# Optimization experiments

Hardware: AMD Instinct MI355X
Metric: run time of the kernel (lower is better)

Reference implementation:

```python
import jax, jax.numpy as jnp
import numpy as np

V = 32000   # vocab
D = 1024    # dim
H = 16      # query heads
HKV = 8     # kv heads (GQA)
DH = D // H # head dim = 64
L = 2       # layers
FF = 3584   # expert hidden dim
E = 8       # experts
K = 2       # top-k
EPS = 1e-5
BASE = 1000000.0
B, S = 1, 2048


def setup_inputs() -> dict:
    key = jax.random.key(0)
    ks = jax.random.split(key, 10)
    s = 0.02
    return {
        "x": jax.random.randint(ks[0], (B, S), 0, V, dtype=jnp.int64) if jax.config.jax_enable_x64 else jax.random.randint(ks[0], (B, S), 0, V),
        "emb": jax.random.normal(ks[1], (V, D), jnp.float32) * s,
        "ln_w": jnp.ones((L, D), jnp.float32),
        "ffln_w": jnp.ones((L, D), jnp.float32),
        "wq": jax.random.normal(ks[2], (L, D, H * DH), jnp.float32) * s,
        "wk": jax.random.normal(ks[3], (L, D, HKV * DH), jnp.float32) * s,
        "wv": jax.random.normal(ks[4], (L, D, HKV * DH), jnp.float32) * s,
        "wo": jax.random.normal(ks[5], (L, H * DH, D), jnp.float32) * s,
        "gate_w": jax.random.normal(ks[6], (L, E, D), jnp.float32) * s,
        "w1": jax.random.normal(ks[7], (L, E, FF, D), jnp.float32) * s,
        "w2": jax.random.normal(ks[8], (L, E, D, FF), jnp.float32) * s,
        "w3": jax.random.normal(ks[9], (L, E, FF, D), jnp.float32) * s,
        "dec_norm_w": jnp.ones((D,), jnp.float32),
    }


def rmsnorm(x, w):
    # LayerNormParameterized(use_mean=False, shift=False) == RMSNorm, pow in fp32
    xf = x.astype(jnp.float32)
    var = jnp.mean(xf * xf, axis=-1, keepdims=True)
    return ((xf * jax.lax.rsqrt(var + EPS)).astype(x.dtype)) * w


def rope(xh, pos):
    # interleaved (complex-pair) rotary embedding, xh: [B, S, h, DH]
    half = DH // 2
    freqs = 1.0 / (BASE ** (jnp.arange(0, half, dtype=jnp.float32) * 2.0 / DH))
    ang = pos[:, None] * freqs[None, :]                       # [S, half]
    cos = jnp.cos(ang)[None, :, None, :]
    sin = jnp.sin(ang)[None, :, None, :]
    x1 = xh[..., 0::2]
    x2 = xh[..., 1::2]
    out = jnp.stack([x1 * cos - x2 * sin, x1 * sin + x2 * cos], axis=-1)
    return out.reshape(xh.shape)


def reference(x, emb, ln_w, ffln_w, wq, wk, wv, wo, gate_w, w1, w2, w3, dec_norm_w):
    h = emb[x]                                                # [B, S, D]
    pos = jnp.arange(S, dtype=jnp.float32)
    causal = jnp.tril(jnp.ones((S, S), bool))[None, None]     # [1,1,S,S]
    scale = 1.0 / np.sqrt(DH).astype(np.float32)
    for i in range(L):
        # --- attention sub-layer ---
        res = h
        xn = rmsnorm(h, ln_w[i])
        q = rope((xn @ wq[i]).reshape(B, S, H, DH), pos)
        k = rope((xn @ wk[i]).reshape(B, S, HKV, DH), pos)
        v = (xn @ wv[i]).reshape(B, S, HKV, DH)
        rep = H // HKV
        k = jnp.repeat(k, rep, axis=2)                        # [B,S,H,DH]
        v = jnp.repeat(v, rep, axis=2)
        scores = jnp.einsum('bqhd,bkhd->bhqk', q, k) * scale
        scores = jnp.where(causal, scores, jnp.float32(-1e9))
        att = jax.nn.softmax(scores, axis=-1)
        o = jnp.einsum('bhqk,bkhd->bqhd', att, v).reshape(B, S, H * DH) @ wo[i]
        h = res + o
        # --- MoE FFN sub-layer ---
        res = h
        xn = rmsnorm(h, ffln_w[i]).reshape(B * S, D)          # [T, D]
        logits = xn @ gate_w[i].T                             # [T, E]
        gates = jax.nn.softmax(logits, axis=-1)
        topw, topi = jax.lax.top_k(gates, K)                  # [T, K]
        topw = topw / jnp.sum(topw, axis=-1, keepdims=True)
        # dense combine weights [T, E] (zero for unselected experts)
        cw = jnp.einsum('tk,tke->te', topw, jax.nn.one_hot(topi, E, dtype=topw.dtype))
        y = jnp.zeros_like(xn)
        for e in range(E):                                    # fixed small expert loop
            ye = (jax.nn.silu(xn @ w1[i, e].T) * (xn @ w3[i, e].T)) @ w2[i, e].T
            y = y + cw[:, e:e + 1] * ye
        h = res + y.reshape(B, S, D)
    return rmsnorm(h, dec_norm_w)
```

## Files before the change

### kernel.cpp

```cpp
#include <hip/hip_runtime.h>

using u16 = unsigned short;
using u32 = unsigned int;

#define TT 2048
#define DM 1024
#define NH 16
#define NKV 8
#define DHD 64
#define FFD 3584
#define NE 8

typedef __bf16 bf16x8 __attribute__((ext_vector_type(8)));
typedef float f32x4 __attribute__((ext_vector_type(4)));

__device__ __forceinline__ u16 f2bf(float x){
  return __builtin_bit_cast(u16, (__bf16)x);
}
__device__ __forceinline__ float bf2f(u16 h){
  return (float)__builtin_bit_cast(__bf16, h);
}
__device__ __forceinline__ f32x4 mfma16(bf16x8 a, bf16x8 b, f32x4 c){
  return __builtin_amdgcn_mfma_f32_16x16x32_bf16(a, b, c, 0, 0, 0);
}
__device__ __forceinline__ uint4 packhi8v(float4 a, float4 b){
  u16 h0=f2bf(a.x),h1=f2bf(a.y),h2=f2bf(a.z),h3=f2bf(a.w);
  u16 h4=f2bf(b.x),h5=f2bf(b.y),h6=f2bf(b.z),h7=f2bf(b.w);
  return make_uint4((u32)h0|((u32)h1<<16),(u32)h2|((u32)h3<<16),
                    (u32)h4|((u32)h5<<16),(u32)h6|((u32)h7<<16));
}
__device__ __forceinline__ uint4 packlo8v(float4 a, float4 b){
  u16 l0=f2bf(a.x-bf2f(f2bf(a.x))),l1=f2bf(a.y-bf2f(f2bf(a.y)));
  u16 l2=f2bf(a.z-bf2f(f2bf(a.z))),l3=f2bf(a.w-bf2f(f2bf(a.w)));
  u16 l4=f2bf(b.x-bf2f(f2bf(b.x))),l5=f2bf(b.y-bf2f(f2bf(b.y)));
  u16 l6=f2bf(b.z-bf2f(f2bf(b.z))),l7=f2bf(b.w-bf2f(f2bf(b.w)));
  return make_uint4((u32)l0|((u32)l1<<16),(u32)l2|((u32)l3<<16),
                    (u32)l4|((u32)l5<<16),(u32)l6|((u32)l7<<16));
}

#define SWZR(r) ((((r)>>1) ^ ((r)>>3)) & 3)
#define SWC(r,c) ((((c) ^ SWZR(r))) * 8)

__device__ __forceinline__ void glds16(const u16* g, u16* l){
  __builtin_amdgcn_global_load_lds(
      (const __attribute__((address_space(1))) void*)g,
      (__attribute__((address_space(3))) void*)l,
      16, 0, 0);
}

__global__ __launch_bounds__(256) void k_embed(const int* __restrict__ x,
    const float* __restrict__ emb, float* __restrict__ h){
  int t = blockIdx.x;
  int d = threadIdx.x * 4;
  float4 v = *reinterpret_cast<const float4*>(emb + (size_t)x[t] * DM + d);
  *reinterpret_cast<float4*>(h + (size_t)t * DM + d) = v;
}

template<int OUTF32>
__global__ __launch_bounds__(256) void k_rmsnorm(const float* __restrict__ in,
    const float* __restrict__ w, u16* __restrict__ oh, u16* __restrict__ ol,
    float* __restrict__ of){
  int t = blockIdx.x;
  int d4 = threadIdx.x * 4;
  float4 xv = *reinterpret_cast<const float4*>(in + (size_t)t * DM + d4);
  float ss = xv.x*xv.x + xv.y*xv.y + xv.z*xv.z + xv.w*xv.w;
#pragma unroll
  for (int m = 1; m < 64; m <<= 1) ss += __shfl_xor(ss, m);
  __shared__ float sred[4];
  if ((threadIdx.x & 63) == 0) sred[threadIdx.x >> 6] = ss;
  __syncthreads();
  float tot = sred[0] + sred[1] + sred[2] + sred[3];
  float r = 1.0f / sqrtf(tot * (1.0f / DM) + 1e-5f);
  float vv[4] = {xv.x, xv.y, xv.z, xv.w};
#pragma unroll
  for (int jj = 0; jj < 4; jj++){
    float xn = (vv[jj] * r) * w[d4 + jj];
    size_t a = (size_t)t * DM + d4 + jj;
    if constexpr (OUTF32){
      of[a] = xn;
    } else {
      u16 hi = f2bf(xn);
      oh[a] = hi;
      ol[a] = f2bf(xn - bf2f(hi));
    }
  }
}

__global__ __launch_bounds__(256) void k_trig(float* __restrict__ ct, float* __restrict__ st){
  int idx = blockIdx.x * 256 + threadIdx.x;
  int j = idx & 31;
  int s = idx >> 5;
  float xe = (float)j * 0.03125f;
  float yf = (float)pow(1.0e6, (double)xe);
  float fr = 1.0f / yf;
  float ang = (float)s * fr;
  double ad = (double)ang;
  ct[idx] = (float)cos(ad);
  st[idx] = (float)sin(ad);
}

template<int NHD>
__global__ __launch_bounds__(256) void k_rope(const float* __restrict__ in,
    const float* __restrict__ ct, const float* __restrict__ st,
    u16* __restrict__ oh, u16* __restrict__ ol){
  int idx = blockIdx.x * 256 + threadIdx.x;
  int j = idx & 31;
  int hd = (idx >> 5) % NHD;
  int s = idx / (32 * NHD);
  size_t base = ((size_t)s * NHD + hd) * 64 + 2 * j;
  float x1 = in[base], x2 = in[base + 1];
  int ti = (s << 5) | j;
  float c  = ct[ti];
  float sn = st[ti];
  float o1 = x1 * c - x2 * sn;
  float o2 = x1 * sn + x2 * c;
  u16 h1 = f2bf(o1), h2 = f2bf(o2);
  oh[base]     = h1; ol[base]     = f2bf(o1 - bf2f(h1));
  oh[base + 1] = h2; ol[base + 1] = f2bf(o2 - bf2f(h2));
}

__global__ __launch_bounds__(256) void k_splitbuf(const float* __restrict__ in,
    u16* __restrict__ oh, u16* __restrict__ ol, int n){
  int i = blockIdx.x * 256 + threadIdx.x;
  if (i < n){
    float x = in[i];
    u16 hi = f2bf(x);
    oh[i] = hi;
    ol[i] = f2bf(x - bf2f(hi));
  }
}

__global__ __launch_bounds__(256) void k_gate(const u16* __restrict__ xh,
    const u16* __restrict__ xl, const float* __restrict__ gw,
    int* __restrict__ topi, float* __restrict__ topw, int* __restrict__ cnt){
  int wv = threadIdx.x >> 6, lane = threadIdx.x & 63;
  int t = blockIdx.x * 4 + wv;
  float x[16];
#pragma unroll
  for (int i = 0; i < 16; i++){
    size_t a = (size_t)t * DM + lane + 64 * i;
    x[i] = bf2f(xh[a]) + bf2f(xl[a]);
  }
  float lgt[8];
#pragma unroll
  for (int e = 0; e < 8; e++){
    float s = 0.f;
#pragma unroll
    for (int i = 0; i < 16; i++) s += x[i] * gw[(size_t)e * DM + lane + 64 * i];
#pragma unroll
    for (int m = 1; m < 64; m <<= 1) s += __shfl_xor(s, m);
    lgt[e] = s;
  }
  float mx = lgt[0];
#pragma unroll
  for (int e = 1; e < 8; e++) mx = fmaxf(mx, lgt[e]);
  float p[8]; float sum = 0.f;
#pragma unroll
  for (int e = 0; e < 8; e++){ p[e] = expf(lgt[e] - mx); sum += p[e]; }
  float g[8];
#pragma unroll
  for (int e = 0; e < 8; e++) g[e] = p[e] / sum;
  int t0 = 0; float b0 = g[0];
#pragma unroll
  for (int e = 1; e < 8; e++) if (g[e] > b0){ b0 = g[e]; t0 = e; }
  int t1 = -1; float b1 = -1.f;
#pragma unroll
  for (int e = 0; e < 8; e++) if (e != t0 && g[e] > b1){ b1 = g[e]; t1 = e; }
  float ssum = b0 + b1;
  float w0 = b0 / ssum, w1 = b1 / ssum;
  if (lane == 0 && t < TT){
    topi[2*t] = t0; topi[2*t+1] = t1;
    topw[2*t] = w0; topw[2*t+1] = w1;
    atomicAdd(&cnt[t0], 1);
    atomicAdd(&cnt[t1], 1);
  }
}

__global__ void k_zero8(int* cnt){ if (threadIdx.x < 8) cnt[threadIdx.x] = 0; }

__global__ void k_scan(const int* __restrict__ cnt, int* __restrict__ offp, int* __restrict__ cur){
  if (threadIdx.x == 0){
    int r = 0;
    for (int e = 0; e < 8; e++){ offp[e] = r; r += cnt[e]; }
  }
  if (threadIdx.x < 8) cur[threadIdx.x] = 0;
}

__global__ __launch_bounds__(256) void k_scatter(const int* __restrict__ topi,
    const float* __restrict__ topw, const int* __restrict__ offp, int* __restrict__ cur,
    int* __restrict__ ftok, float* __restrict__ fwt){
  int t = blockIdx.x * 256 + threadIdx.x;
  if (t < TT){
#pragma unroll
    for (int j = 0; j < 2; j++){
      int e = topi[2*t + j];
      int p = atomicAdd(&cur[e], 1);
      ftok[offp[e] + p] = t;
      fwt[offp[e] + p] = topw[2*t + j];
    }
  }
}

#define GLDSA(BUF, KK) do { \
    glds16(Ah + gaA0 + (KK), (u16*)&Ash[BUF][awr0][0]); \
    glds16(Ah + gaA1 + (KK), (u16*)&Ash[BUF][awr1][0]); \
    if constexpr (SPLIT){ \
      glds16(Al + gaA0 + (KK), (u16*)&Asl[BUF][awr0][0]); \
      glds16(Al + gaA1 + (KK), (u16*)&Asl[BUF][awr1][0]); \
    } \
  } while(0)

#define GPRELOADB(S, KK) do { \
    if constexpr (BLAYOUT == 0){ \
      const float* bp_ = Bw + (size_t)(n0 + br0) * K + (KK) + cb8; \
      S##B0 = *reinterpret_cast<const float4*>(bp_); \
      S##B1 = *reinterpret_cast<const float4*>(bp_ + 4); \
      if constexpr (TN == 128){ \
        const float* bp2_ = Bw + (size_t)(n0 + br1) * K + (KK) + cb8; \
        S##B2 = *reinterpret_cast<const float4*>(bp2_); \
        S##B3 = *reinterpret_cast<const float4*>(bp2_ + 4); \
      } \
      if constexpr (DUAL){ \
        const float* bq_ = B3w + (size_t)(n0 + br0) * K + (KK) + cb8; \
        S##B2 = *reinterpret_cast<const float4*>(bq_); \
        S##B3 = *reinterpret_cast<const float4*>(bq_ + 4); \
      } \
    } else { \
      S##B0 = *reinterpret_cast<const float4*>(Bw + (size_t)((KK) + kk1) * Nq + n0 + nn1); \
      S##B1 = *reinterpret_cast<const float4*>(Bw + (size_t)((KK) + 16 + kk1) * Nq + n0 + nn1); \
    } \
  } while(0)

#define GSTOREB(S) do { \
    if constexpr (BLAYOUT == 0){ \
      *reinterpret_cast<uint4*>(&Bh1[br0][swB0]) = packhi8v(S##B0, S##B1); \
      if constexpr (SPLIT) *reinterpret_cast<uint4*>(&Bl1[br0][swB0]) = packlo8v(S##B0, S##B1); \
      if constexpr (TN == 128){ \
        *reinterpret_cast<uint4*>(&Bh1[br1][swB1]) = packhi8v(S##B2, S##B3); \
        if constexpr (SPLIT) *reinterpret_cast<uint4*>(&Bl1[br1][swB1]) = packlo8v(S##B2, S##B3); \
      } \
      if constexpr (DUAL){ \
        *reinterpret_cast<uint4*>(&Bh3[br0][swB0]) = packhi8v(S##B2, S##B3); \
        if constexpr (SPLIT) *reinterpret_cast<uint4*>(&Bl3[br0][swB0]) = packlo8v(S##B2, S##B3); \
      } \
    } else { \
      const float* q0 = reinterpret_cast<const float*>(&S##B0); \
      const float* q1 = reinterpret_cast<const float*>(&S##B1); \
      const int ch0 = kk1 >> 3, off0 = kk1 & 7; \
      _Pragma("unroll") \
      for (int j = 0; j < 4; j++){ \
        int row = nn1 + j; \
        int c0 = SWC(row, ch0) + off0; \
        int c1 = SWC(row, ch0 + 2) + off0; \
        u16 h0 = f2bf(q0[j]); \
        Bh1[row][c0] = h0; \
        if constexpr (SPLIT) Bl1[row][c0] = f2bf(q0[j] - bf2f(h0)); \
        u16 h1 = f2bf(q1[j]); \
        Bh1[row][c1] = h1; \
        if constexpr (SPLIT) Bl1[row][c1] = f2bf(q1[j] - bf2f(h1)); \
      } \
    } \
  } while(0)

#define WAITN() do { \
    if constexpr (NBLD == 4) asm volatile("s_waitcnt vmcnt(4) lgkmcnt(0)" ::: "memory"); \
    else                     asm volatile("s_waitcnt vmcnt(2) lgkmcnt(0)" ::: "memory"); \
  } while(0)
#define WAIT0() asm volatile("s_waitcnt vmcnt(0) lgkmcnt(0)" ::: "memory")

#define MFMA_PHASE(CURB) do { \
    bf16x8 af[4], afl[4]; \
    _Pragma("unroll") \
    for (int m = 0; m < 4; m++){ \
      int Ra = wr*64 + m*16 + lr; \
      int sa = SWC(Ra, lg); \
      af[m] = *reinterpret_cast<const bf16x8*>(&Ash[CURB][Ra][sa]); \
      if constexpr (SPLIT) \
        afl[m] = *reinterpret_cast<const bf16x8*>(&Asl[CURB][Ra][sa]); \
    } \
    _Pragma("unroll") \
    for (int n = 0; n < NF; n++){ \
      int Rb = wc*(TN/2) + n*16 + lr; \
      int sb = SWC(Rb, lg); \
      bf16x8 b1 = *reinterpret_cast<const bf16x8*>(&Bh1[Rb][sb]); \
      _Pragma("unroll") \
      for (int m = 0; m < 4; m++) acc[m][n] = mfma16(af[m], b1, acc[m][n]); \
      if constexpr (SPLIT){ \
        bf16x8 bl = *reinterpret_cast<const bf16x8*>(&Bl1[Rb][sb]); \
        _Pragma("unroll") \
        for (int m = 0; m < 4; m++){ \
          acc[m][n] = mfma16(af[m], bl, acc[m][n]); \
          acc[m][n] = mfma16(afl[m], b1, acc[m][n]); \
        } \
      } \
      if constexpr (DUAL){ \
        bf16x8 b3 = *reinterpret_cast<const bf16x8*>(&Bh3[Rb][sb]); \
        _Pragma("unroll") \
        for (int m = 0; m < 4; m++) acc3[m][n] = mfma16(af[m], b3, acc3[m][n]); \
        if constexpr (SPLIT){ \
          bf16x8 b3l = *reinterpret_cast<const bf16x8*>(&Bl3[Rb][sb]); \
          _Pragma("unroll") \
          for (int m = 0; m < 4; m++){ \
            acc3[m][n] = mfma16(af[m], b3l, acc3[m][n]); \
            acc3[m][n] = mfma16(afl[m], b3, acc3[m][n]); \
          } \
        } \
      } \
    } \
  } while(0)

template<int BLAYOUT, int EPI, int SPLIT, int DUAL, int TN, int KS>
__global__ __launch_bounds__(256) void k_gemm(
    const u16* __restrict__ Ah, const u16* __restrict__ Al,
    const float* __restrict__ Bw, const float* __restrict__ B3w,
    const float* __restrict__ Bw2, const float* __restrict__ Bw3,
    size_t strideB, int N, int K,
    float* __restrict__ Cf, int ldc,
    float* __restrict__ Cf2, float* __restrict__ Cf3,
    u16* __restrict__ Ch, u16* __restrict__ Cl,
    const int* __restrict__ cntp, const int* __restrict__ offp,
    const int* __restrict__ ftok, const float* __restrict__ fwt)
{
  static_assert(!(DUAL && TN != 64), "DUAL uses TN=64");
  static_assert(!(BLAYOUT == 1 && TN != 64), "BLAYOUT=1 uses TN=64");
  constexpr int NBLD = (BLAYOUT == 0 && (DUAL || TN == 128)) ? 4 : 2;
  int cnt = TT, off = 0, ks = 0;
  if constexpr (EPI == 2 || EPI == 3){
    int e = blockIdx.z / KS;
    ks = blockIdx.z % KS;
    cnt = cntp[e]; off = offp[e];
    if ((int)blockIdx.y * 128 >= cnt) return;
    Bw += (size_t)e * strideB;
    if constexpr (DUAL) B3w += (size_t)e * strideB;
  } else if constexpr (KS > 1){
    ks = blockIdx.z;
  }
  __shared__ u16 Ash[2][128][32];
  __shared__ u16 Asl[SPLIT ? 2 : 1][SPLIT ? 128 : 1][32];
  __shared__ u16 Bh1[TN][32];
  __shared__ u16 Bl1[SPLIT ? TN : 1][32];
  __shared__ u16 Bh3[DUAL ? TN : 1][32];
  __shared__ u16 Bl3[(DUAL && SPLIT) ? TN : 1][32];

  const int tid = threadIdx.x;
  const int m0 = blockIdx.y * 128;

  int n0, Nq = N, ldq = ldc;
  float* Cq = Cf;
  if constexpr (EPI == 4){
    int bx = blockIdx.x;
    if (bx < 16){       n0 = bx * 64;        Nq = 1024; ldq = 1024; Cq = Cf;  }
    else if (bx < 24){  n0 = (bx - 16) * 64; Nq = 512;  ldq = 512;  Cq = Cf2; Bw = Bw2; }
    else {              n0 = (bx - 24) * 64; Nq = 512;  ldq = 512;  Cq = Cf3; Bw = Bw3; }
  } else {
    n0 = blockIdx.x * TN;
  }

  const int wid = tid >> 6, lane = tid & 63;
  const int wr = wid >> 1, wc = wid & 1;
  const int lr = lane & 15, lg = lane >> 4;
  constexpr int NF = TN / 32;

  const int awr0 = wid * 32;
  const int awr1 = wid * 32 + 16;
  const int rA0 = awr0 + (lane >> 2);
  const int rA1 = awr1 + (lane >> 2);
  const int cA0 = (lane & 3) ^ SWZR(rA0);
  const int cA1 = (lane & 3) ^ SWZR(rA1);
  int grA0, grA1;
  {
    int g0 = m0 + rA0, g1 = m0 + rA1;
    if constexpr (EPI == 2){
      grA0 = ftok[off + (g0 < cnt ? g0 : cnt - 1)];
      grA1 = ftok[off + (g1 < cnt ? g1 : cnt - 1)];
    } else if constexpr (EPI == 3){
      grA0 = off + (g0 < cnt ? g0 : cnt - 1);
      grA1 = off + (g1 < cnt ? g1 : cnt - 1);
    } else {
      grA0 = g0; grA1 = g1;
    }
  }
  const size_t gaA0 = (size_t)grA0 * K + cA0 * 8;
  const size_t gaA1 = (size_t)grA1 * K + cA1 * 8;

  const int br0 = tid >> 2;
  const int br1 = br0 + 64;
  const int cb8 = (tid & 3) * 8;
  const int swB0 = SWC(br0, tid & 3), swB1 = SWC(br1, tid & 3);
  const int kk1 = tid >> 4;
  const int nn1 = (tid & 15) * 4;

  f32x4 acc[4][NF];
  f32x4 acc3[DUAL ? 4 : 1][NF];
#pragma unroll
  for (int m = 0; m < 4; m++)
#pragma unroll
    for (int n = 0; n < NF; n++){
      acc[m][n] = f32x4{0.f,0.f,0.f,0.f};
      if constexpr (DUAL) acc3[m][n] = f32x4{0.f,0.f,0.f,0.f};
    }

  float4 aB0{}, aB1{}, aB2{}, aB3{};
  float4 bB0{}, bB1{}, bB2{}, bB3{};

  const int kbeg = ks * (K / KS);
  const int kend = kbeg + (K / KS);

  GLDSA(0, kbeg);
  GPRELOADB(a, kbeg);
  if (kbeg + 32 < kend) GPRELOADB(b, kbeg + 32);
  int cur = 0;
  for (int k0 = kbeg; k0 < kend; k0 += 64){
    {
      const bool pre = (k0 + 64 < kend);
      GSTOREB(a);
      if (pre) WAITN(); else WAIT0();
      __builtin_amdgcn_s_barrier();
      if (k0 + 32 < kend) GLDSA(cur ^ 1, k0 + 32);
      if (pre) GPRELOADB(a, k0 + 64);
      MFMA_PHASE(cur);
      __builtin_amdgcn_s_barrier();
      cur ^= 1;
    }
    if (k0 + 32 < kend){
      const bool pre = (k0 + 96 < kend);
      GSTOREB(b);
      if (pre) WAITN(); else WAIT0();
      __builtin_amdgcn_s_barrier();
      if (k0 + 64 < kend) GLDSA(cur ^ 1, k0 + 64);
      if (pre) GPRELOADB(b, k0 + 96);
      MFMA_PHASE(cur);
      __builtin_amdgcn_s_barrier();
      cur ^= 1;
    }
  }

#pragma unroll
  for (int m = 0; m < 4; m++)
#pragma unroll
    for (int n = 0; n < NF; n++)
#pragma unroll
      for (int r = 0; r < 4; r++){
        int row = m0 + wr*64 + m*16 + lg*4 + r;
        int col = n0 + wc*(TN/2) + n*16 + lr;
        float v = acc[m][n][r];
        if constexpr (EPI == 0){
          Cf[(size_t)row * ldc + col] = v;
        } else if constexpr (EPI == 1){
          if constexpr (KS > 1) atomicAdd(&Cf[(size_t)row * ldc + col], v);
          else                  Cf[(size_t)row * ldc + col] += v;
        } else if constexpr (EPI == 2){
          if (row < cnt){
            float a3 = acc3[m][n][r];
            float s = v / (1.0f + expf(-v));
            float y = s * a3;
            u16 hi = f2bf(y);
            size_t oa = (size_t)(off + row) * ldc + col;
            Ch[oa] = hi;
            Cl[oa] = f2bf(y - bf2f(hi));
          }
        } else if constexpr (EPI == 3){
          if (row < cnt){
            int tok = ftok[off + row];
            float wgt = fwt[off + row];
            atomicAdd(&Cf[(size_t)tok * ldc + col], wgt * v);
          }
        } else {
          if constexpr (KS > 1) atomicAdd(&Cq[(size_t)row * ldq + col], v);
          else                  Cq[(size_t)row * ldq + col] = v;
        }
      }
}

__global__ __launch_bounds__(256) void k_attn(
    const u16* __restrict__ qh, const u16* __restrict__ ql,
    const u16* __restrict__ kh, const u16* __restrict__ kl,
    const u16* __restrict__ vh, const u16* __restrict__ vl,
    u16* __restrict__ aoh, u16* __restrict__ aol)
{
  const int h  = blockIdx.y;
  const int q0 = blockIdx.x * 64;
  const int hk = h >> 1;
  const int tid = threadIdx.x;
  const int wv = tid >> 6, lane = tid & 63;
  const int lr = lane & 15, lg = lane >> 4;
  const int qw0 = q0 + wv * 16;

  __shared__ u16 Khs[32][72], Kls[32][72];
  __shared__ u16 Vhs[64][40], Vls[64][40];
  __shared__ u16 Phs[4][16][40], Pls[4][16][40];

  bf16x8 qfh[2], qfl[2];
#pragma unroll
  for (int dc = 0; dc < 2; dc++){
    size_t qa = ((size_t)(qw0 + lr) * NH + h) * 64 + dc*32 + lg*8;
    qfh[dc] = *reinterpret_cast<const bf16x8*>(qh + qa);
    qfl[dc] = *reinterpret_cast<const bf16x8*>(ql + qa);
  }
  f32x4 oacc[4];
  float mrun[4], lrun[4];
#pragma unroll
  for (int r = 0; r < 4; r++){ mrun[r] = -1e30f; lrun[r] = 0.f; }
#pragma unroll
  for (int g = 0; g < 4; g++) oacc[g] = f32x4{0.f,0.f,0.f,0.f};

  const int nt = q0 / 32 + 2;
  for (int kt = 0; kt < nt; kt++){
    int kg = kt * 32;
    {
      int kk = tid >> 3, c8 = (tid & 7) * 8;
      size_t ka = ((size_t)(kg + kk) * NKV + hk) * 64 + c8;
      *reinterpret_cast<uint4*>(&Khs[kk][c8]) = *reinterpret_cast<const uint4*>(kh + ka);
      *reinterpret_cast<uint4*>(&Kls[kk][c8]) = *reinterpret_cast<const uint4*>(kl + ka);
      uint4 v1 = *reinterpret_cast<const uint4*>(vh + ka);
      uint4 v2 = *reinterpret_cast<const uint4*>(vl + ka);
      const u16* p1 = reinterpret_cast<const u16*>(&v1);
      const u16* p2 = reinterpret_cast<const u16*>(&v2);
#pragma unroll
      for (int j = 0; j < 8; j++){ Vhs[c8 + j][kk] = p1[j]; Vls[c8 + j][kk] = p2[j]; }
    }
    __syncthreads();

    f32x4 sc[2];
    sc[0] = f32x4{0.f,0.f,0.f,0.f};
    sc[1] = f32x4{0.f,0.f,0.f,0.f};
#pragma unroll
    for (int c = 0; c < 2; c++){
#pragma unroll
      for (int dc = 0; dc < 2; dc++){
        bf16x8 bh = *reinterpret_cast<const bf16x8*>(&Khs[c*16 + lr][dc*32 + lg*8]);
        bf16x8 bl = *reinterpret_cast<const bf16x8*>(&Kls[c*16 + lr][dc*32 + lg*8]);
        sc[c] = mfma16(qfh[dc], bh, sc[c]);
        sc[c] = mfma16(qfh[dc], bl, sc[c]);
        sc[c] = mfma16(qfl[dc], bh, sc[c]);
      }
    }
    float pnew[2][4], corr[4];
#pragma unroll
    for (int r = 0; r < 4; r++){
      int row = qw0 + lg*4 + r;
      float s0 = (kg + lr      <= row) ? sc[0][r] * 0.125f : -1e30f;
      float s1 = (kg + 16 + lr <= row) ? sc[1][r] * 0.125f : -1e30f;
      float tm = fmaxf(s0, s1);
#pragma unroll
      for (int m = 1; m < 16; m <<= 1) tm = fmaxf(tm, __shfl_xor(tm, m));
      float mnew = fmaxf(mrun[r], tm);
      corr[r] = expf(mrun[r] - mnew);
      float p0 = expf(s0 - mnew);
      float p1 = expf(s1 - mnew);
      pnew[0][r] = p0; pnew[1][r] = p1;
      float sm = p0 + p1;
#pragma unroll
      for (int m = 1; m < 16; m <<= 1) sm += __shfl_xor(sm, m);
      lrun[r] = lrun[r] * corr[r] + sm;
      mrun[r] = mnew;
    }
#pragma unroll
    for (int g = 0; g < 4; g++){
      f32x4 t = oacc[g];
#pragma unroll
      for (int r = 0; r < 4; r++) t[r] *= corr[r];
      oacc[g] = t;
    }
#pragma unroll
    for (int c = 0; c < 2; c++)
#pragma unroll
      for (int r = 0; r < 4; r++){
        float p = pnew[c][r];
        u16 hi = f2bf(p);
        Phs[wv][lg*4 + r][c*16 + lr] = hi;
        Pls[wv][lg*4 + r][c*16 + lr] = f2bf(p - bf2f(hi));
      }
    asm volatile("s_waitcnt lgkmcnt(0)" ::: "memory");
    __builtin_amdgcn_sched_barrier(0);
    bf16x8 pah = *reinterpret_cast<const bf16x8*>(&Phs[wv][lr][lg*8]);
    bf16x8 pal = *reinterpret_cast<const bf16x8*>(&Pls[wv][lr][lg*8]);
#pragma unroll
    for (int g = 0; g < 4; g++){
      bf16x8 vb1 = *reinterpret_cast<const bf16x8*>(&Vhs[g*16 + lr][lg*8]);
      bf16x8 vb2 = *reinterpret_cast<const bf16x8*>(&Vls[g*16 + lr][lg*8]);
      oacc[g] = mfma16(pah, vb1, oacc[g]);
      oacc[g] = mfma16(pah, vb2, oacc[g]);
      oacc[g] = mfma16(pal, vb1, oacc[g]);
    }
    __syncthreads();
  }
#pragma unroll
  for (int g = 0; g < 4; g++)
#pragma unroll
    for (int r = 0; r < 4; r++){
      int row = qw0 + lg*4 + r;
      float v = oacc[g][r] / lrun[r];
      u16 hi = f2bf(v);
      size_t oa = ((size_t)row * NH + h) * 64 + g*16 + lr;
      aoh[oa] = hi;
      aol[oa] = f2bf(v - bf2f(hi));
    }
}

extern "C" void kernel_launch(void* const* d_in, const int* in_sizes, int n_in,
                              void* d_out, int out_size, void* d_ws, size_t ws_size,
                              hipStream_t stream){
  const int*   x     = (const int*)d_in[0];
  const float* emb   = (const float*)d_in[1];
  const float* lnw   = (const float*)d_in[2];
  const float* fflnw = (const float*)d_in[3];
  const float* wq    = (const float*)d_in[4];
  const float* wk    = (const float*)d_in[5];
  const float* wvp   = (const float*)d_in[6];
  const float* wo    = (const float*)d_in[7];
  const float* gw    = (const float*)d_in[8];
  const float* w1    = (const float*)d_in[9];
  const float* w2    = (const float*)d_in[10];
  const float* w3    = (const float*)d_in[11];
  const float* dnw   = (const float*)d_in[12];
  float* out = (float*)d_out;

  char* p = (char*)d_ws;
  auto alloc = [&](size_t bytes)->char*{
    char* r = p; p += (bytes + 255) & ~(size_t)255; return r;
  };
  float* h    = (float*)alloc((size_t)TT * DM * 4);
  float* qbuf = (float*)alloc((size_t)TT * 1024 * 4);
  float* kbuf = (float*)alloc((size_t)TT * 512 * 4);
  float* vbuf = (float*)alloc((size_t)TT * 512 * 4);
  u16* xnh = (u16*)alloc((size_t)TT * DM * 2);
  u16* xnl = (u16*)alloc((size_t)TT * DM * 2);
  u16* qhb = (u16*)alloc((size_t)TT * 1024 * 2);
  u16* qlb = (u16*)alloc((size_t)TT * 1024 * 2);
  u16* khb = (u16*)alloc((size_t)TT * 512 * 2);
  u16* klb = (u16*)alloc((size_t)TT * 512 * 2);
  u16* vhb = (u16*)alloc((size_t)TT * 512 * 2);
  u16* vlb = (u16*)alloc((size_t)TT * 512 * 2);
  u16* aoh = (u16*)alloc((size_t)TT * 1024 * 2);
  u16* aol = (u16*)alloc((size_t)TT * 1024 * 2);
  u16* acth = (u16*)alloc((size_t)2 * TT * FFD * 2);
  u16* actl = (u16*)alloc((size_t)2 * TT * FFD * 2);
  int*   topi = (int*)alloc((size_t)2 * TT * 4);
  float* topw = (float*)alloc((size_t)2 * TT * 4);
  int* cnt  = (int*)alloc(64);
  int* offe = (int*)alloc(64);
  int* cur  = (int*)alloc(64);
  int*   ftok = (int*)alloc((size_t)2 * TT * 4);
  float* fwt  = (float*)alloc((size_t)2 * TT * 4);
  float* ctab = (float*)aoh;
  float* stab = (float*)aol;

  k_embed<<<TT, 256, 0, stream>>>(x, emb, h);

  for (int i = 0; i < 2; i++){
    const float* wq_i = wq + (size_t)i * DM * 1024;
    const float* wk_i = wk + (size_t)i * DM * 512;
    const float* wv_i = wvp + (size_t)i * DM * 512;
    const float* wo_i = wo + (size_t)i * 1024 * DM;
    const float* w1_i = w1 + (size_t)i * NE * FFD * DM;
    const float* w2_i = w2 + (size_t)i * NE * DM * FFD;
    const float* w3_i = w3 + (size_t)i * NE * FFD * DM;

    k_rmsnorm<0><<<TT, 256, 0, stream>>>(h, lnw + i * DM, xnh, xnl, nullptr);

    hipMemsetAsync(qbuf, 0, (size_t)TT * 1024 * 4, stream);
    hipMemsetAsync(kbuf, 0, (size_t)TT * 512 * 4, stream);
    hipMemsetAsync(vbuf, 0, (size_t)TT * 512 * 4, stream);
    k_gemm<1,4,1,0,64,2><<<dim3(32,16,2), 256, 0, stream>>>(xnh, xnl,
        wq_i, nullptr, wk_i, wv_i, 0, 1024, DM,
        qbuf, 1024, kbuf, vbuf, nullptr, nullptr, nullptr, nullptr, nullptr, nullptr);

    k_trig<<<TT * 32 / 256, 256, 0, stream>>>(ctab, stab);
    k_rope<16><<<4096, 256, 0, stream>>>(qbuf, ctab, stab, qhb, qlb);
    k_rope<8><<<2048, 256, 0, stream>>>(kbuf, ctab, stab, khb, klb);
    k_splitbuf<<<4096, 256, 0, stream>>>(vbuf, vhb, vlb, TT * 512);

    k_attn<<<dim3(32,16,1), 256, 0, stream>>>(qhb, qlb, khb, klb, vhb, vlb, aoh, aol);

    k_gemm<1,1,1,0,64,2><<<dim3(16,16,2), 256, 0, stream>>>(aoh, aol,
        wo_i, nullptr, nullptr, nullptr, 0, DM, 1024,
        h, DM, nullptr, nullptr, nullptr, nullptr, nullptr, nullptr, nullptr, nullptr);

    k_rmsnorm<0><<<TT, 256, 0, stream>>>(h, fflnw + i * DM, xnh, xnl, nullptr);

    k_zero8<<<1, 64, 0, stream>>>(cnt);
    k_gate<<<TT/4, 256, 0, stream>>>(xnh, xnl, gw + (size_t)i * NE * DM, topi, topw, cnt);
    k_scan<<<1, 64, 0, stream>>>(cnt, offe, cur);
    k_scatter<<<8, 256, 0, stream>>>(topi, topw, offe, cur, ftok, fwt);

    if (i == 0){
      k_gemm<0,2,1,1,64,1><<<dim3(FFD/64,16,8), 256, 0, stream>>>(xnh, xnl,
          w1_i, w3_i, nullptr, nullptr, (size_t)FFD * DM, FFD, DM,
          nullptr, FFD, nullptr, nullptr, acth, actl, cnt, offe, ftok, fwt);
      k_gemm<0,3,1,0,128,4><<<dim3(DM/128,16,32), 256, 0, stream>>>(acth, actl,
          w2_i, nullptr, nullptr, nullptr, (size_t)DM * FFD, DM, FFD,
          h, DM, nullptr, nullptr, nullptr, nullptr, cnt, offe, ftok, fwt);
    } else {
      k_gemm<0,2,0,1,64,1><<<dim3(FFD/64,16,8), 256, 0, stream>>>(xnh, xnl,
          w1_i, w3_i, nullptr, nullptr, (size_t)FFD * DM, FFD, DM,
          nullptr, FFD, nullptr, nullptr, acth, actl, cnt, offe, ftok, fwt);
      k_gemm<0,3,0,0,128,4><<<dim3(DM/128,16,32), 256, 0, stream>>>(acth, actl,
          w2_i, nullptr, nullptr, nullptr, (size_t)DM * FFD, DM, FFD,
          h, DM, nullptr, nullptr, nullptr, nullptr, cnt, offe, ftok, fwt);
    }
  }

  k_rmsnorm<1><<<TT, 256, 0, stream>>>(h, dnw, nullptr, nullptr, out);
}
```

Before: 1.691 ms.

## Add deep 64-k staged GEMM pipeline with double B buffers for non-split MoE

Adds a DEEP template mode that loads two 32-wide k slices of A and B into LDS per barrier pair, using four A buffers and two B buffers. This halves the barriers per k in the layer-1 MoE GEMMs. The non-deep path is simplified to a single 32-k step with a full vmcnt(0) wait each iteration. That removes the partial-wait overlap the old loop had and may expose global-load latency in the split-precision GEMMs.

```diff
diff --git a/kernel.cpp b/kernel.cpp
--- a/kernel.cpp
+++ b/kernel.cpp
@@ -231,16 +231,16 @@
     } \
   } while(0)
 
-#define GSTOREB(S) do { \
+#define GSTOREB(S, BB) do { \
     if constexpr (BLAYOUT == 0){ \
-      *reinterpret_cast<uint4*>(&Bh1[br0][swB0]) = packhi8v(S##B0, S##B1); \
+      *reinterpret_cast<uint4*>(&Bh1[BB][br0][swB0]) = packhi8v(S##B0, S##B1); \
       if constexpr (SPLIT) *reinterpret_cast<uint4*>(&Bl1[br0][swB0]) = packlo8v(S##B0, S##B1); \
       if constexpr (TN == 128){ \
-        *reinterpret_cast<uint4*>(&Bh1[br1][swB1]) = packhi8v(S##B2, S##B3); \
+        *reinterpret_cast<uint4*>(&Bh1[BB][br1][swB1]) = packhi8v(S##B2, S##B3); \
         if constexpr (SPLIT) *reinterpret_cast<uint4*>(&Bl1[br1][swB1]) = packlo8v(S##B2, S##B3); \
       } \
       if constexpr (DUAL){ \
-        *reinterpret_cast<uint4*>(&Bh3[br0][swB0]) = packhi8v(S##B2, S##B3); \
+        *reinterpret_cast<uint4*>(&Bh3[BB][br0][swB0]) = packhi8v(S##B2, S##B3); \
         if constexpr (SPLIT) *reinterpret_cast<uint4*>(&Bl3[br0][swB0]) = packlo8v(S##B2, S##B3); \
       } \
     } else { \
@@ -253,22 +253,16 @@
         int c0 = SWC(row, ch0) + off0; \
         int c1 = SWC(row, ch0 + 2) + off0; \
         u16 h0 = f2bf(q0[j]); \
-        Bh1[row][c0] = h0; \
+        Bh1[BB][row][c0] = h0; \
         if constexpr (SPLIT) Bl1[row][c0] = f2bf(q0[j] - bf2f(h0)); \
         u16 h1 = f2bf(q1[j]); \
-        Bh1[row][c1] = h1; \
+        Bh1[BB][row][c1] = h1; \
         if constexpr (SPLIT) Bl1[row][c1] = f2bf(q1[j] - bf2f(h1)); \
       } \
     } \
   } while(0)
 
-#define WAITN() do { \
-    if constexpr (NBLD == 4) asm volatile("s_waitcnt vmcnt(4) lgkmcnt(0)" ::: "memory"); \
-    else                     asm volatile("s_waitcnt vmcnt(2) lgkmcnt(0)" ::: "memory"); \
-  } while(0)
-#define WAIT0() asm volatile("s_waitcnt vmcnt(0) lgkmcnt(0)" ::: "memory")
-
-#define MFMA_PHASE(CURB) do { \
+#define MFMA_PHASE(CURB, BB) do { \
     bf16x8 af[4], afl[4]; \
     _Pragma("unroll") \
     for (int m = 0; m < 4; m++){ \
@@ -282,7 +276,7 @@
     for (int n = 0; n < NF; n++){ \
       int Rb = wc*(TN/2) + n*16 + lr; \
       int sb = SWC(Rb, lg); \
-      bf16x8 b1 = *reinterpret_cast<const bf16x8*>(&Bh1[Rb][sb]); \
+      bf16x8 b1 = *reinterpret_cast<const bf16x8*>(&Bh1[BB][Rb][sb]); \
       _Pragma("unroll") \
       for (int m = 0; m < 4; m++) acc[m][n] = mfma16(af[m], b1, acc[m][n]); \
       if constexpr (SPLIT){ \
@@ -294,7 +288,7 @@
         } \
       } \
       if constexpr (DUAL){ \
-        bf16x8 b3 = *reinterpret_cast<const bf16x8*>(&Bh3[Rb][sb]); \
+        bf16x8 b3 = *reinterpret_cast<const bf16x8*>(&Bh3[BB][Rb][sb]); \
         _Pragma("unroll") \
         for (int m = 0; m < 4; m++) acc3[m][n] = mfma16(af[m], b3, acc3[m][n]); \
         if constexpr (SPLIT){ \
@@ -309,7 +303,7 @@
     } \
   } while(0)
 
-template<int BLAYOUT, int EPI, int SPLIT, int DUAL, int TN, int KS>
+template<int BLAYOUT, int EPI, int SPLIT, int DUAL, int TN, int KS, int DEEP>
 __global__ __launch_bounds__(256) void k_gemm(
     const u16* __restrict__ Ah, const u16* __restrict__ Al,
     const float* __restrict__ Bw, const float* __restrict__ B3w,
@@ -323,7 +317,8 @@
 {
   static_assert(!(DUAL && TN != 64), "DUAL uses TN=64");
   static_assert(!(BLAYOUT == 1 && TN != 64), "BLAYOUT=1 uses TN=64");
-  constexpr int NBLD = (BLAYOUT == 0 && (DUAL || TN == 128)) ? 4 : 2;
+  static_assert(!(DEEP && SPLIT), "DEEP only for SPLIT=0 (A-LDS budget)");
+  static_assert(!(DEEP && BLAYOUT == 1), "DEEP only for BLAYOUT=0");
   int cnt = TT, off = 0, ks = 0;
   if constexpr (EPI == 2 || EPI == 3){
     int e = blockIdx.z / KS;
@@ -335,11 +330,11 @@
   } else if constexpr (KS > 1){
     ks = blockIdx.z;
   }
-  __shared__ u16 Ash[2][128][32];
+  __shared__ u16 Ash[DEEP ? 4 : 2][128][32];
   __shared__ u16 Asl[SPLIT ? 2 : 1][SPLIT ? 128 : 1][32];
-  __shared__ u16 Bh1[TN][32];
+  __shared__ u16 Bh1[DEEP ? 2 : 1][TN][32];
   __shared__ u16 Bl1[SPLIT ? TN : 1][32];
-  __shared__ u16 Bh3[DUAL ? TN : 1][32];
+  __shared__ u16 Bh3[DEEP ? 2 : 1][DUAL ? TN : 1][32];
   __shared__ u16 Bl3[(DUAL && SPLIT) ? TN : 1][32];
 
   const int tid = threadIdx.x;
@@ -406,30 +401,41 @@
   const int kbeg = ks * (K / KS);
   const int kend = kbeg + (K / KS);
 
-  GLDSA(0, kbeg);
-  GPRELOADB(a, kbeg);
-  if (kbeg + 32 < kend) GPRELOADB(b, kbeg + 32);
-  int cur = 0;
-  for (int k0 = kbeg; k0 < kend; k0 += 64){
-    {
-      const bool pre = (k0 + 64 < kend);
-      GSTOREB(a);
-      if (pre) WAITN(); else WAIT0();
+  if constexpr (DEEP){
+    GLDSA(0, kbeg);
+    GLDSA(1, kbeg + 32);
+    GPRELOADB(a, kbeg);
+    GPRELOADB(b, kbeg + 32);
+    int cur = 0;
+    for (int k0 = kbeg; k0 < kend; k0 += 64){
+      GSTOREB(a, 0);
+      GSTOREB(b, 1);
+      asm volatile("s_waitcnt vmcnt(0) lgkmcnt(0)" ::: "memory");
       __builtin_amdgcn_s_barrier();
-      if (k0 + 32 < kend) GLDSA(cur ^ 1, k0 + 32);
-      if (pre) GPRELOADB(a, k0 + 64);
-      MFMA_PHASE(cur);
+      if (k0 + 64 < kend){
+        GLDSA(cur ^ 2, k0 + 64);
+        GLDSA((cur ^ 2) + 1, k0 + 96);
+        GPRELOADB(a, k0 + 64);
+        GPRELOADB(b, k0 + 96);
+      }
+      MFMA_PHASE(cur, 0);
+      MFMA_PHASE(cur + 1, 1);
       __builtin_amdgcn_s_barrier();
-      cur ^= 1;
-    }
-    if (k0 + 32 < kend){
-      const bool pre = (k0 + 96 < kend);
-      GSTOREB(b);
-      if (pre) WAITN(); else WAIT0();
+      cur ^= 2;
+    }
+  } else {
+    GLDSA(0, kbeg);
+    GPRELOADB(a, kbeg);
+    int cur = 0;
+    for (int k0 = kbeg; k0 < kend; k0 += 32){
+      GSTOREB(a, 0);
+      asm volatile("s_waitcnt vmcnt(0) lgkmcnt(0)" ::: "memory");
       __builtin_amdgcn_s_barrier();
-      if (k0 + 64 < kend) GLDSA(cur ^ 1, k0 + 64);
-      if (pre) GPRELOADB(b, k0 + 96);
-      MFMA_PHASE(cur);
+      if (k0 + 32 < kend){
+        GLDSA(cur ^ 1, k0 + 32);
+        GPRELOADB(a, k0 + 32);
+      }
+      MFMA_PHASE(cur, 0);
       __builtin_amdgcn_s_barrier();
       cur ^= 1;
     }
@@ -662,7 +668,7 @@
     hipMemsetAsync(qbuf, 0, (size_t)TT * 1024 * 4, stream);
     hipMemsetAsync(kbuf, 0, (size_t)TT * 512 * 4, stream);
     hipMemsetAsync(vbuf, 0, (size_t)TT * 512 * 4, stream);
-    k_gemm<1,4,1,0,64,2><<<dim3(32,16,2), 256, 0, stream>>>(xnh, xnl,
+    k_gemm<1,4,1,0,64,2,0><<<dim3(32,16,2), 256, 0, stream>>>(xnh, xnl,
         wq_i, nullptr, wk_i, wv_i, 0, 1024, DM,
         qbuf, 1024, kbuf, vbuf, nullptr, nullptr, nullptr, nullptr, nullptr, nullptr);
 
@@ -673,7 +679,7 @@
 
     k_attn<<<dim3(32,16,1), 256, 0, stream>>>(qhb, qlb, khb, klb, vhb, vlb, aoh, aol);
 
-    k_gemm<1,1,1,0,64,2><<<dim3(16,16,2), 256, 0, stream>>>(aoh, aol,
+    k_gemm<1,1,1,0,64,2,0><<<dim3(16,16,2), 256, 0, stream>>>(aoh, aol,
         wo_i, nullptr, nullptr, nullptr, 0, DM, 1024,
         h, DM, nullptr, nullptr, nullptr, nullptr, nullptr, nullptr, nullptr, nullptr);
 
@@ -685,17 +691,17 @@
     k_scatter<<<8, 256, 0, stream>>>(topi, topw, offe, cur, ftok, fwt);
 
     if (i == 0){
-      k_gemm<0,2,1,1,64,1><<<dim3(FFD/64,16,8), 256, 0, stream>>>(xnh, xnl,
+      k_gemm<0,2,1,1,64,1,0><<<dim3(FFD/64,16,8), 256, 0, stream>>>(xnh, xnl,
           w1_i, w3_i, nullptr, nullptr, (size_t)FFD * DM, FFD, DM,
           nullptr, FFD, nullptr, nullptr, acth, actl, cnt, offe, ftok, fwt);
-      k_gemm<0,3,1,0,128,4><<<dim3(DM/128,16,32), 256, 0, stream>>>(acth, actl,
+      k_gemm<0,3,1,0,128,4,0><<<dim3(DM/128,16,32), 256, 0, stream>>>(acth, actl,
           w2_i, nullptr, nullptr, nullptr, (size_t)DM * FFD, DM, FFD,
           h, DM, nullptr, nullptr, nullptr, nullptr, cnt, offe, ftok, fwt);
     } else {
-      k_gemm<0,2,0,1,64,1><<<dim3(FFD/64,16,8), 256, 0, stream>>>(xnh, xnl,
+      k_gemm<0,2,0,1,64,1,1><<<dim3(FFD/64,16,8), 256, 0, stream>>>(xnh, xnl,
           w1_i, w3_i, nullptr, nullptr, (size_t)FFD * DM, FFD, DM,
           nullptr, FFD, nullptr, nullptr, acth, actl, cnt, offe, ftok, fwt);
-      k_gemm<0,3,0,0,128,4><<<dim3(DM/128,16,32), 256, 0, stream>>>(acth, actl,
+      k_gemm<0,3,0,0,128,4,1><<<dim3(DM/128,16,32), 256, 0, stream>>>(acth, actl,
           w2_i, nullptr, nullptr, nullptr, (size_t)DM * FFD, DM, FFD,
           h, DM, nullptr, nullptr, nullptr, nullptr, cnt, offe, ftok, fwt);
     }
```

After: 1.469 ms. -13.1%, faster.
